# Kernel tuning notes

Measured on AMD Instinct MI355X. Metric: run time of the kernel, lower is better.

The kernel has to match this reference:

```python
import jax, jax.numpy as jnp
import numpy as np

NEG_SLOPE = 0.2
EPS = 1e-16

def gat_conv(x, edge_index, W, a_src, a_dst, b):
    # x: [N, Fin], W: [Fin, C], a_src/a_dst: [C], b: [C]
    N = x.shape[0]
    src, dst = edge_index[0], edge_index[1]
    h = x @ W                                  # [N, C]
    alpha_s = h @ a_src                        # [N]
    alpha_d = h @ a_dst                        # [N]
    e = alpha_s[src] + alpha_d[dst]            # [E]
    e = jnp.where(e > 0, e, NEG_SLOPE * e)     # LeakyReLU(0.2)
    # ragged softmax over incoming edges of each dst node
    m = jax.ops.segment_max(e, dst, num_segments=N)       # [N]
    p = jnp.exp(e - m[dst])                                # [E]
    s = jax.ops.segment_sum(p, dst, num_segments=N)        # [N]
    alpha = p / (s[dst] + EPS)                             # [E]
    out = jax.ops.segment_sum(alpha[:, None] * h[src], dst, num_segments=N)
    return out + b

def setup_inputs() -> dict:
    key = jax.random.key(0)
    ks = jax.random.split(key, 10)
    N, Fin, H, C, E = 50000, 128, 64, 64, 800000
    x = jax.random.normal(ks[0], (N, Fin), dtype=jnp.float32)
    edge_index = jax.random.randint(ks[1], (2, E), 0, N, dtype=jnp.int64)
    sc1 = 1.0 / np.sqrt(Fin)
    sc2 = 1.0 / np.sqrt(H)
    W1 = jax.random.normal(ks[2], (Fin, H), dtype=jnp.float32) * sc1
    a_src1 = jax.random.normal(ks[3], (H,), dtype=jnp.float32) * sc2
    a_dst1 = jax.random.normal(ks[4], (H,), dtype=jnp.float32) * sc2
    b1 = jnp.zeros((H,), dtype=jnp.float32)
    W2 = jax.random.normal(ks[5], (H, C), dtype=jnp.float32) * sc2
    a_src2 = jax.random.normal(ks[6], (C,), dtype=jnp.float32) * sc2
    a_dst2 = jax.random.normal(ks[7], (C,), dtype=jnp.float32) * sc2
    b2 = jnp.zeros((C,), dtype=jnp.float32)
    return {"x": x, "edge_index": edge_index, "W1": W1, "a_src1": a_src1,
            "a_dst1": a_dst1, "b1": b1, "W2": W2, "a_src2": a_src2,
            "a_dst2": a_dst2, "b2": b2}

def reference(x, edge_index, W1, a_src1, a_dst1, b1, W2, a_src2, a_dst2, b2):
    h = gat_conv(x, edge_index, W1, a_src1, a_dst1, b1)
    h = jax.nn.relu(h)
    out = gat_conv(h, edge_index, W2, a_src2, a_dst2, b2)
    return out
```

## Files before the change

kernel.cpp:

```cpp
#include <hip/hip_runtime.h>
#include <cstddef>

constexpr int FIN = 128;
constexpr int EPB = 2048;
constexpr int BSH = 7;
constexpr int NPB = 128;
constexpr int PACK_SH = 25;

typedef _Float16 half4 __attribute__((ext_vector_type(4)));
typedef _Float16 half8 __attribute__((ext_vector_type(8)));
typedef float floatx4 __attribute__((ext_vector_type(4)));

__device__ __forceinline__ int block_scan_tot(int v, int tid, int* wsums,
                                              int* tot) {
    int lane = tid & 63, w = tid >> 6;
    int x = v;
#pragma unroll
    for (int off = 1; off < 64; off <<= 1) {
        int y = __shfl_up(x, off, 64);
        if (lane >= off) x += y;
    }
    if (lane == 63) wsums[w] = x;
    __syncthreads();
    int add = 0;
#pragma unroll
    for (int i = 0; i < 4; ++i) add += (i < w) ? wsums[i] : 0;
    *tot = wsums[0] + wsums[1] + wsums[2] + wsums[3];
    return x + add - v;
}

template <int K, typename XT>
__device__ __forceinline__
void gemm_mfma_body(const XT* __restrict__ X, const float* __restrict__ W,
                    const float* __restrict__ ASRC, const float* __restrict__ ADST,
                    _Float16* __restrict__ Hh, float* __restrict__ AS,
                    float* __restrict__ AD, int N, int blk,
                    _Float16* Xh, _Float16* WT) {
    constexpr int LDH = K + 8;
    const int tid = threadIdx.x;
    const int nb = blk * 64;

    if constexpr (sizeof(XT) == 4) {
        constexpr int QPR = K / 4;
        for (int i = tid; i < 64 * QPR; i += 256) {
            int r = i / QPR, q = i % QPR;
            float4 v = make_float4(0.f, 0.f, 0.f, 0.f);
            if (nb + r < N) v = *(const float4*)(X + (size_t)(nb + r) * K + 4 * q);
            half4 h; h[0] = (_Float16)v.x; h[1] = (_Float16)v.y;
            h[2] = (_Float16)v.z; h[3] = (_Float16)v.w;
            *(half4*)(Xh + r * LDH + 4 * q) = h;
        }
    } else {
        constexpr int OPR = K / 8;
        for (int i = tid; i < 64 * OPR; i += 256) {
            int r = i / OPR, o = i % OPR;
            half8 v = {};
            if (nb + r < N) v = *(const half8*)(X + (size_t)(nb + r) * K + 8 * o);
            *(half8*)(Xh + r * LDH + 8 * o) = v;
        }
    }
    for (int i = tid; i < 64 * (K / 4); i += 256) {
        int n = i & 63, kg = i >> 6;
        half4 h;
#pragma unroll
        for (int j = 0; j < 4; ++j)
            h[j] = (_Float16)W[(4 * kg + j) * 64 + n];
        *(half4*)(WT + n * LDH + 4 * kg) = h;
    }
    __syncthreads();

    const int l = tid & 63;
    const int r0 = (tid >> 6) * 16;
    const int n16 = l & 15, quad = l >> 4;

    floatx4 acc[4];
#pragma unroll
    for (int nt = 0; nt < 4; ++nt) acc[nt] = (floatx4){0.f, 0.f, 0.f, 0.f};

#pragma unroll
    for (int k0 = 0; k0 < K; k0 += 32) {
        half8 a = *(const half8*)(Xh + (r0 + n16) * LDH + k0 + quad * 8);
#pragma unroll
        for (int nt = 0; nt < 4; ++nt) {
            half8 b = *(const half8*)(WT + (nt * 16 + n16) * LDH + k0 + quad * 8);
            acc[nt] = __builtin_amdgcn_mfma_f32_16x16x32_f16(a, b, acc[nt], 0, 0, 0);
        }
    }

    float pa[4] = {0.f, 0.f, 0.f, 0.f}, pd[4] = {0.f, 0.f, 0.f, 0.f};
#pragma unroll
    for (int nt = 0; nt < 4; ++nt) {
        float as_v = ASRC[nt * 16 + n16], ad_v = ADST[nt * 16 + n16];
#pragma unroll
        for (int reg = 0; reg < 4; ++reg) {
            pa[reg] += acc[nt][reg] * as_v;
            pd[reg] += acc[nt][reg] * ad_v;
        }
    }
#pragma unroll
    for (int off = 1; off < 16; off <<= 1) {
#pragma unroll
        for (int reg = 0; reg < 4; ++reg) {
            pa[reg] += __shfl_xor(pa[reg], off, 64);
            pd[reg] += __shfl_xor(pd[reg], off, 64);
        }
    }
    if (n16 == 0) {
#pragma unroll
        for (int reg = 0; reg < 4; ++reg) {
            int row = nb + r0 + quad * 4 + reg;
            if (row < N) { AS[row] = pa[reg]; AD[row] = pd[reg]; }
        }
    }

#pragma unroll
    for (int nt = 0; nt < 4; ++nt)
#pragma unroll
        for (int reg = 0; reg < 4; ++reg)
            Xh[(r0 + quad * 4 + reg) * LDH + nt * 16 + n16] = (_Float16)acc[nt][reg];
    {
        int r = r0 + (l >> 2);
        int o = (l & 3) * 16;
        if (nb + r < N) {
            half8 v0 = *(const half8*)(Xh + r * LDH + o);
            half8 v1 = *(const half8*)(Xh + r * LDH + o + 8);
            *(half8*)(Hh + (size_t)(nb + r) * 64 + o) = v0;
            *(half8*)(Hh + (size_t)(nb + r) * 64 + o + 8) = v1;
        }
    }
}

__global__ __launch_bounds__(256)
void gemm1_and_count(const float* __restrict__ X, const float* __restrict__ W,
                     const float* __restrict__ ASRC, const float* __restrict__ ADST,
                     _Float16* __restrict__ Hh, float* __restrict__ AS,
                     float* __restrict__ AD, int N,
                     const int* __restrict__ dst, int E, int nblk, int nbuck,
                     int* __restrict__ cnts, int* __restrict__ ticket) {
    constexpr int K = FIN, LDH = K + 8;
    __shared__ _Float16 Xh[64 * LDH];
    __shared__ _Float16 WT[64 * LDH];

    const int tid = threadIdx.x;
    if ((int)blockIdx.x < nblk) {
        int* hist = (int*)Xh;
        if (blockIdx.x == 0 && tid == 0) *ticket = 0;
        for (int i = tid; i < nbuck; i += 256) hist[i] = 0;
        __syncthreads();
        int e0 = blockIdx.x * EPB;
        int e1 = min(e0 + EPB, E);
        for (int e = e0 + tid; e < e1; e += 256)
            atomicAdd(&hist[dst[e] >> BSH], 1);
        __syncthreads();
        for (int i = tid; i < nbuck; i += 256)
            cnts[blockIdx.x * nbuck + i] = hist[i];
        return;
    }
    gemm_mfma_body<K, float>(X, W, ASRC, ADST, Hh, AS, AD, N,
                             blockIdx.x - nblk, Xh, WT);
}

template <int K, typename XT>
__global__ __launch_bounds__(256)
void gemm_feat(const XT* __restrict__ X, const float* __restrict__ W,
               const float* __restrict__ ASRC, const float* __restrict__ ADST,
               _Float16* __restrict__ Hh, float* __restrict__ AS,
               float* __restrict__ AD, int N) {
    constexpr int LDH = K + 8;
    __shared__ _Float16 Xh[64 * LDH];
    __shared__ _Float16 WT[64 * LDH];
    gemm_mfma_body<K, XT>(X, W, ASRC, ADST, Hh, AS, AD, N, blockIdx.x, Xh, WT);
}

__global__ __launch_bounds__(256)
void bucket_colscan_fused(int* __restrict__ cnts, int nblk, int nbuck,
                          int* __restrict__ btotal, int* __restrict__ bbase,
                          int* __restrict__ ticket) {
    __shared__ int wsums[4];
    __shared__ int lastflag;
    int b = blockIdx.x;
    int tid = threadIdx.x;
    int carry = 0;
    for (int c0 = 0; c0 < nblk; c0 += 256) {
        int t = c0 + tid;
        int v = (t < nblk) ? cnts[t * nbuck + b] : 0;
        int tot;
        int e = block_scan_tot(v, tid, wsums, &tot);
        if (t < nblk) cnts[t * nbuck + b] = e + carry;
        carry += tot;
        __syncthreads();
    }
    if (tid == 0) {
        atomicExch(&btotal[b], carry);
        int old = atomicAdd(ticket, 1);
        lastflag = (old == nbuck - 1);
    }
    __syncthreads();
    if (!lastflag) return;
    int i0 = 2 * tid, i1 = 2 * tid + 1;
    int v0 = (i0 < nbuck) ? atomicAdd(&btotal[i0], 0) : 0;
    int v1 = (i1 < nbuck) ? atomicAdd(&btotal[i1], 0) : 0;
    __syncthreads();
    int tot2;
    int e2 = block_scan_tot(v0 + v1, tid, wsums, &tot2);
    if (i0 <= nbuck) bbase[i0] = e2;
    if (i1 <= nbuck) bbase[i1] = e2 + v0;
}

__global__ __launch_bounds__(256)
void bucket_scatter(const int* __restrict__ src, const int* __restrict__ dst,
                    int E, int nbuck, const int* __restrict__ cnts,
                    const int* __restrict__ bbase, int* __restrict__ ebuck) {
    __shared__ int cur[512];
    int tid = threadIdx.x;
    for (int i = tid; i < nbuck; i += 256)
        cur[i] = bbase[i] + cnts[blockIdx.x * nbuck + i];
    __syncthreads();
    int e0 = blockIdx.x * EPB;
    int e1 = min(e0 + EPB, E);
    for (int e = e0 + tid; e < e1; e += 256) {
        int d = dst[e];
        int p = atomicAdd(&cur[d >> BSH], 1);
        ebuck[p] = ((d & (NPB - 1)) << PACK_SH) | src[e];
    }
}

__global__ __launch_bounds__(256)
void bucket_to_csr(const int* __restrict__ ebuck, const int* __restrict__ bbase,
                   int N, int E, int* __restrict__ row_ptr,
                   int* __restrict__ csr_src) {
    __shared__ int hist[NPB];
    __shared__ int cur[NPB];
    __shared__ int wsums[4];
    int b = blockIdx.x, tid = threadIdx.x;
    int nstart = b << BSH;
    int base = bbase[b], endp = bbase[b + 1];
    if (tid < NPB) hist[tid] = 0;
    __syncthreads();
    for (int e = base + tid; e < endp; e += 256)
        atomicAdd(&hist[((unsigned)ebuck[e]) >> PACK_SH], 1);
    __syncthreads();
    int v = (tid < NPB) ? hist[tid] : 0;
    int tot;
    int excl = block_scan_tot(v, tid, wsums, &tot);
    if (tid < NPB) {
        cur[tid] = excl;
        if (nstart + tid < N) row_ptr[nstart + tid] = base + excl;
    }
    if (b == 0 && tid == 0) row_ptr[N] = E;
    __syncthreads();
    for (int e = base + tid; e < endp; e += 256) {
        int pv = ebuck[e];
        int p = atomicAdd(&cur[((unsigned)pv) >> PACK_SH], 1);
        csr_src[base + p] = pv & ((1 << PACK_SH) - 1);
    }
}

template <typename OT>
__global__ __launch_bounds__(256)
void gat_aggregate(const _Float16* __restrict__ Hh, const float* __restrict__ AS,
                   const float* __restrict__ AD, const int* __restrict__ row_ptr,
                   const int* __restrict__ csr_src, const float* __restrict__ bias,
                   OT* __restrict__ OUT, int N, int relu) {
    const int lane = threadIdx.x & 63;
    const int n = blockIdx.x * 4 + (threadIdx.x >> 6);
    if (n >= N) return;

    const int base = row_ptr[n], end = row_ptr[n + 1];
    const int cnt = end - base;
    const float adn = AD[n];

    if (cnt > 64) {
        float m = -INFINITY;
        for (int c0 = base; c0 < end; c0 += 64) {
            int c = min(64, end - c0);
            float e = -INFINITY;
            if (lane < c) {
                int sr = csr_src[c0 + lane];
                float t = AS[sr] + adn;
                e = t > 0.f ? t : 0.2f * t;
            }
#pragma unroll
            for (int off = 32; off > 0; off >>= 1) e = fmaxf(e, __shfl_xor(e, off, 64));
            m = fmaxf(m, e);
        }
        float s = 0.f, acc = 0.f;
        for (int c0 = base; c0 < end; c0 += 64) {
            int c = min(64, end - c0);
            int srcl = 0;
            float p = 0.f;
            if (lane < c) {
                srcl = csr_src[c0 + lane];
                float t = AS[srcl] + adn;
                t = t > 0.f ? t : 0.2f * t;
                p = __expf(t - m);
            }
            float cs = p;
#pragma unroll
            for (int off = 32; off > 0; off >>= 1) cs += __shfl_xor(cs, off, 64);
            s += cs;
            for (int j = 0; j < c; ++j)
                acc += __shfl(p, j, 64) *
                       (float)Hh[(size_t)__shfl(srcl, j, 64) * 64 + lane];
        }
        float o = acc * (1.f / (s + 1e-16f)) + bias[lane];
        if (relu) o = fmaxf(o, 0.f);
        OUT[(size_t)n * 64 + lane] = (OT)o;
        return;
    }

    int srcl = 0;
    float el = 0.f;
    if (lane < cnt) {
        srcl = csr_src[base + lane];
        float e = AS[srcl] + adn;
        el = e > 0.f ? e : 0.2f * e;
    }
    float p = (lane < cnt) ? __expf(el) : 0.f;
    float s = p;
#pragma unroll
    for (int off = 32; off > 0; off >>= 1) s += __shfl_xor(s, off, 64);
    const float inv = 1.f / (s + 1e-16f);

    const int eg = lane >> 3;
    const int c8 = (lane & 7) * 8;

    float acc[8], acc2[8];
#pragma unroll
    for (int t = 0; t < 8; ++t) { acc[t] = 0.f; acc2[t] = 0.f; }

    int j = 0;
    for (; j + 16 <= cnt; j += 16) {
        int iA = j + eg, iB = j + 8 + eg;
        int sA = __shfl(srcl, iA, 64), sB = __shfl(srcl, iB, 64);
        float aA = __shfl(p, iA, 64),  aB = __shfl(p, iB, 64);
        half8 hA = *(const half8*)(Hh + (size_t)sA * 64 + c8);
        half8 hB = *(const half8*)(Hh + (size_t)sB * 64 + c8);
#pragma unroll
        for (int t = 0; t < 8; ++t) {
            acc[t]  += aA * (float)hA[t];
            acc2[t] += aB * (float)hB[t];
        }
    }
    for (; j < cnt; j += 8) {
        int iA = j + eg;
        int sA = __shfl(srcl, iA, 64);
        float aA = __shfl(p, iA, 64);
        half8 hA = *(const half8*)(Hh + (size_t)sA * 64 + c8);
#pragma unroll
        for (int t = 0; t < 8; ++t) acc[t] += aA * (float)hA[t];
    }
#pragma unroll
    for (int t = 0; t < 8; ++t) acc[t] += acc2[t];
#pragma unroll
    for (int off = 8; off <= 32; off <<= 1)
#pragma unroll
        for (int t = 0; t < 8; ++t) acc[t] += __shfl_xor(acc[t], off, 64);

    if (lane < 8) {
        float4 b0 = *(const float4*)(bias + c8);
        float4 b1 = *(const float4*)(bias + c8 + 4);
        float o[8];
        o[0] = acc[0] * inv + b0.x; o[1] = acc[1] * inv + b0.y;
        o[2] = acc[2] * inv + b0.z; o[3] = acc[3] * inv + b0.w;
        o[4] = acc[4] * inv + b1.x; o[5] = acc[5] * inv + b1.y;
        o[6] = acc[6] * inv + b1.z; o[7] = acc[7] * inv + b1.w;
        if (relu) {
#pragma unroll
            for (int t = 0; t < 8; ++t) o[t] = fmaxf(o[t], 0.f);
        }
        if constexpr (sizeof(OT) == 2) {
            half8 hv;
#pragma unroll
            for (int t = 0; t < 8; ++t) hv[t] = (_Float16)o[t];
            *(half8*)((_Float16*)OUT + (size_t)n * 64 + c8) = hv;
        } else {
            *(float4*)((float*)OUT + (size_t)n * 64 + c8) =
                make_float4(o[0], o[1], o[2], o[3]);
            *(float4*)((float*)OUT + (size_t)n * 64 + c8 + 4) =
                make_float4(o[4], o[5], o[6], o[7]);
        }
    }
}

extern "C" void kernel_launch(void* const* d_in, const int* in_sizes, int n_in,
                              void* d_out, int out_size, void* d_ws, size_t ws_size,
                              hipStream_t stream) {
    const float* x    = (const float*)d_in[0];
    const int*   ei   = (const int*)d_in[1];
    const float* W1   = (const float*)d_in[2];
    const float* as1w = (const float*)d_in[3];
    const float* ad1w = (const float*)d_in[4];
    const float* b1   = (const float*)d_in[5];
    const float* W2   = (const float*)d_in[6];
    const float* as2w = (const float*)d_in[7];
    const float* ad2w = (const float*)d_in[8];
    const float* b2   = (const float*)d_in[9];
    float* out = (float*)d_out;

    const int N = in_sizes[0] / FIN;
    const int E = in_sizes[1] / 2;
    const int* esrc = ei;
    const int* edst = ei + E;

    const int nbuck = (N + NPB - 1) >> BSH;
    const int nblk  = (E + EPB - 1) / EPB;

    char* wp8 = (char*)d_ws;
    _Float16* Hh  = (_Float16*)wp8;  wp8 += (size_t)N * 64 * 2;
    _Float16* R1h = (_Float16*)wp8;  wp8 += (size_t)N * 64 * 2;
    float* AS1 = (float*)wp8;        wp8 += (size_t)N * 4;
    float* AD1 = (float*)wp8;        wp8 += (size_t)N * 4;
    float* AS2 = (float*)wp8;        wp8 += (size_t)N * 4;
    float* AD2 = (float*)wp8;        wp8 += (size_t)N * 4;
    int* row_ptr = (int*)wp8;        wp8 += (size_t)(N + 1) * 4;
    int* csr     = (int*)wp8;        wp8 += (size_t)E * 4;
    int* ebuck   = (int*)wp8;        wp8 += (size_t)E * 4;
    int* cnts    = (int*)wp8;        wp8 += (size_t)nblk * nbuck * 4;
    int* btotal  = (int*)wp8;        wp8 += (size_t)nbuck * 4;
    int* bbase   = (int*)wp8;        wp8 += (size_t)(nbuck + 1) * 4;
    int* ticket  = (int*)wp8;        wp8 += 4;

    const int nbG = (N + 63) / 64;
    const int nbAgg = (N + 3) / 4;

    hipLaunchKernelGGL(gemm1_and_count, dim3(nblk + nbG), dim3(256), 0, stream,
                       x, W1, as1w, ad1w, Hh, AS1, AD1, N,
                       edst, E, nblk, nbuck, cnts, ticket);
    hipLaunchKernelGGL(bucket_colscan_fused, dim3(nbuck), dim3(256), 0, stream,
                       cnts, nblk, nbuck, btotal, bbase, ticket);
    hipLaunchKernelGGL(bucket_scatter, dim3(nblk), dim3(256), 0, stream,
                       esrc, edst, E, nbuck, cnts, bbase, ebuck);
    hipLaunchKernelGGL(bucket_to_csr, dim3(nbuck), dim3(256), 0, stream,
                       ebuck, bbase, N, E, row_ptr, csr);
    hipLaunchKernelGGL(gat_aggregate<_Float16>, dim3(nbAgg), dim3(256), 0,
                       stream, Hh, AS1, AD1, row_ptr, csr, b1, R1h, N, 1);
    hipLaunchKernelGGL((gemm_feat<64, _Float16>), dim3(nbG), dim3(256), 0, stream,
                       R1h, W2, as2w, ad2w, Hh, AS2, AD2, N);
    hipLaunchKernelGGL(gat_aggregate<float>, dim3(nbAgg), dim3(256), 0,
                       stream, Hh, AS2, AD2, row_ptr, csr, b2, out, N, 0);
}
```

Baseline: 186.9 us.

## Process two nodes per wavefront in GAT aggregation when degrees are small

The aggregation kernel now assigns two destination nodes to each 64-lane wavefront, one per 32-lane half, whenever both nodes have at most 32 incoming edges. That fast path computes the softmax without the separate max pass, using exp directly, and accumulates features with 32-wide shuffles. When either node exceeds 32 edges, the wave falls back to the original one-node routine for each node in turn. The aim is to cut lane idling, since the average in-degree here is about 16, at the cost of more branch complexity and skipping max subtraction, which could overflow for large logits.

```diff
diff --git a/kernel.cpp b/kernel.cpp
--- a/kernel.cpp
+++ b/kernel.cpp
@@ -257,16 +257,11 @@
 }
 
 template <typename OT>
-__global__ __launch_bounds__(256)
-void gat_aggregate(const _Float16* __restrict__ Hh, const float* __restrict__ AS,
-                   const float* __restrict__ AD, const int* __restrict__ row_ptr,
-                   const int* __restrict__ csr_src, const float* __restrict__ bias,
-                   OT* __restrict__ OUT, int N, int relu) {
-    const int lane = threadIdx.x & 63;
-    const int n = blockIdx.x * 4 + (threadIdx.x >> 6);
-    if (n >= N) return;
-
-    const int base = row_ptr[n], end = row_ptr[n + 1];
+__device__ __forceinline__
+void agg_one_node(const _Float16* __restrict__ Hh, const float* __restrict__ AS,
+                  const float* __restrict__ AD, const int* __restrict__ csr_src,
+                  const float* __restrict__ bias, OT* __restrict__ OUT,
+                  int n, int base, int end, int lane, int relu) {
     const int cnt = end - base;
     const float adn = AD[n];
 
@@ -358,6 +353,108 @@
         for (int t = 0; t < 8; ++t) acc[t] += __shfl_xor(acc[t], off, 64);
 
     if (lane < 8) {
+        float4 b0 = *(const float4*)(bias + c8);
+        float4 b1 = *(const float4*)(bias + c8 + 4);
+        float o[8];
+        o[0] = acc[0] * inv + b0.x; o[1] = acc[1] * inv + b0.y;
+        o[2] = acc[2] * inv + b0.z; o[3] = acc[3] * inv + b0.w;
+        o[4] = acc[4] * inv + b1.x; o[5] = acc[5] * inv + b1.y;
+        o[6] = acc[6] * inv + b1.z; o[7] = acc[7] * inv + b1.w;
+        if (relu) {
+#pragma unroll
+            for (int t = 0; t < 8; ++t) o[t] = fmaxf(o[t], 0.f);
+        }
+        if constexpr (sizeof(OT) == 2) {
+            half8 hv;
+#pragma unroll
+            for (int t = 0; t < 8; ++t) hv[t] = (_Float16)o[t];
+            *(half8*)((_Float16*)OUT + (size_t)n * 64 + c8) = hv;
+        } else {
+            *(float4*)((float*)OUT + (size_t)n * 64 + c8) =
+                make_float4(o[0], o[1], o[2], o[3]);
+            *(float4*)((float*)OUT + (size_t)n * 64 + c8 + 4) =
+                make_float4(o[4], o[5], o[6], o[7]);
+        }
+    }
+}
+
+template <typename OT>
+__global__ __launch_bounds__(256)
+void gat_aggregate(const _Float16* __restrict__ Hh, const float* __restrict__ AS,
+                   const float* __restrict__ AD, const int* __restrict__ row_ptr,
+                   const int* __restrict__ csr_src, const float* __restrict__ bias,
+                   OT* __restrict__ OUT, int N, int relu) {
+    const int lane = threadIdx.x & 63;
+    const int half = lane >> 5;
+    const int l32  = lane & 31;
+    const int pair0 = blockIdx.x * 8 + (threadIdx.x >> 6) * 2;
+    if (pair0 >= N) return;
+    const int n = pair0 + half;
+
+    int base = 0, end = 0;
+    if (n < N) { base = row_ptr[n]; end = row_ptr[n + 1]; }
+    const int cnt = end - base;
+
+    if (!__all(cnt <= 32)) {
+        int baseA = __shfl(base, 0, 64),  endA = __shfl(end, 0, 64);
+        int baseB = __shfl(base, 32, 64), endB = __shfl(end, 32, 64);
+        agg_one_node(Hh, AS, AD, csr_src, bias, OUT, pair0, baseA, endA, lane, relu);
+        if (pair0 + 1 < N)
+            agg_one_node(Hh, AS, AD, csr_src, bias, OUT, pair0 + 1, baseB, endB,
+                         lane, relu);
+        return;
+    }
+
+    const float adn = (n < N) ? AD[n] : 0.f;
+    int srcl = 0;
+    float p = 0.f;
+    if (l32 < cnt) {
+        srcl = csr_src[base + l32];
+        float e = AS[srcl] + adn;
+        e = e > 0.f ? e : 0.2f * e;
+        p = __expf(e);
+    }
+    float s = p;
+#pragma unroll
+    for (int off = 16; off > 0; off >>= 1) s += __shfl_xor(s, off, 64);
+    const float inv = 1.f / (s + 1e-16f);
+
+    const int eg = l32 >> 3;
+    const int c8 = (l32 & 7) * 8;
+
+    float acc[8], acc2[8];
+#pragma unroll
+    for (int t = 0; t < 8; ++t) { acc[t] = 0.f; acc2[t] = 0.f; }
+
+    int j = 0;
+    for (; j + 8 <= cnt; j += 8) {
+        int iA = j + eg, iB = j + 4 + eg;
+        int sA = __shfl(srcl, iA, 32), sB = __shfl(srcl, iB, 32);
+        float aA = __shfl(p, iA, 32),  aB = __shfl(p, iB, 32);
+        half8 hA = *(const half8*)(Hh + (size_t)sA * 64 + c8);
+        half8 hB = *(const half8*)(Hh + (size_t)sB * 64 + c8);
+#pragma unroll
+        for (int t = 0; t < 8; ++t) {
+            acc[t]  += aA * (float)hA[t];
+            acc2[t] += aB * (float)hB[t];
+        }
+    }
+    for (; j < cnt; j += 4) {
+        int iA = j + eg;
+        int sA = __shfl(srcl, iA, 32);
+        float aA = __shfl(p, iA, 32);
+        half8 hA = *(const half8*)(Hh + (size_t)sA * 64 + c8);
+#pragma unroll
+        for (int t = 0; t < 8; ++t) acc[t] += aA * (float)hA[t];
+    }
+#pragma unroll
+    for (int t = 0; t < 8; ++t) acc[t] += acc2[t];
+#pragma unroll
+    for (int t = 0; t < 8; ++t) acc[t] += __shfl_xor(acc[t], 8, 64);
+#pragma unroll
+    for (int t = 0; t < 8; ++t) acc[t] += __shfl_xor(acc[t], 16, 64);
+
+    if (l32 < 8 && n < N) {
         float4 b0 = *(const float4*)(bias + c8);
         float4 b1 = *(const float4*)(bias + c8 + 4);
         float o[8];
@@ -422,7 +519,7 @@
     int* ticket  = (int*)wp8;        wp8 += 4;
 
     const int nbG = (N + 63) / 64;
-    const int nbAgg = (N + 3) / 4;
+    const int nbAgg = (N + 7) / 8;
 
     hipLaunchKernelGGL(gemm1_and_count, dim3(nblk + nbG), dim3(256), 0, stream,
                        x, W1, as1w, ad1w, Hh, AS1, AD1, N,
```

Measured after the change: 174.7 us. -6.5%, faster.
